# Kernel tuning notes

Hardware: AMD Instinct MI355X
Metric: run time of the kernel (lower is better)

Reference implementation:

```python
import jax, jax.numpy as jnp
import numpy as np

DIM = 64
NUM_NODES = 64
SEQ_LEN = 256
BATCH = 64


def setup_inputs() -> dict:
    key = jax.random.key(0)
    ks = jax.random.split(key, 8)
    D = DIM
    x = jax.random.normal(ks[0], (SEQ_LEN, BATCH, NUM_NODES, D), dtype=jnp.float32)
    mask = jnp.ones((SEQ_LEN,), dtype=jnp.int32)
    # msg MLP: Linear(3D -> D) + GELU
    lim_msg = 1.0 / np.sqrt(3 * D)
    msg_W = jax.random.uniform(ks[1], (D, 3 * D), minval=-lim_msg, maxval=lim_msg, dtype=jnp.float32)
    msg_b = jax.random.uniform(ks[2], (D,), minval=-lim_msg, maxval=lim_msg, dtype=jnp.float32)
    # GRUCell(input=D, hidden=D); torch init U(-1/sqrt(hidden), 1/sqrt(hidden))
    lim_g = 1.0 / np.sqrt(D)
    W_ih = jax.random.uniform(ks[3], (3 * D, D), minval=-lim_g, maxval=lim_g, dtype=jnp.float32)
    W_hh = jax.random.uniform(ks[4], (3 * D, D), minval=-lim_g, maxval=lim_g, dtype=jnp.float32)
    b_ih = jax.random.uniform(ks[5], (3 * D,), minval=-lim_g, maxval=lim_g, dtype=jnp.float32)
    b_hh = jax.random.uniform(ks[6], (3 * D,), minval=-lim_g, maxval=lim_g, dtype=jnp.float32)
    # TimeEncode params
    basis_freq = jnp.asarray(1.0 / 10.0 ** np.linspace(0, 9, D), dtype=jnp.float32)
    phase = jnp.zeros((D,), dtype=jnp.float32)
    return {"x": x, "mask": mask, "msg_W": msg_W, "msg_b": msg_b,
            "W_ih": W_ih, "W_hh": W_hh, "b_ih": b_ih, "b_hh": b_hh,
            "basis_freq": basis_freq, "phase": phase}


def _forward(x, mask, msg_W, msg_b, W_ih, W_hh, b_ih, b_hh, basis_freq, phase):
    T, B, C, D = x.shape
    # TimeEncode: cos(t * freq + phase) -> [T, D]
    ts = jnp.arange(T, dtype=jnp.float32)[:, None]
    t_enc = jnp.cos(ts * basis_freq[None, :] + phase[None, :])
    # init_func == 'mean': mean over time -> [B, C, D] -> [B*C, D]
    s0 = jnp.mean(x, axis=0).reshape(B * C, D)
    # time_range = arange(T) * mask (gather indices)
    tr = jnp.arange(T) * mask.astype(jnp.int32)
    x_seq = x[tr].reshape(T, B * C, D)      # gathered timesteps
    te_seq = t_enc[tr]                       # [T, D]

    def step(s, inp):
        xt, tt = inp                        # xt: [B*C, D], tt: [D]
        tt_b = jnp.broadcast_to(tt[None, :], xt.shape)
        cat = jnp.concatenate([xt, s, tt_b], axis=-1)  # [B*C, 3D]
        msg = jax.nn.gelu(cat @ msg_W.T + msg_b, approximate=False)
        # GRUCell (torch gate order: r, z, n)
        gi = msg @ W_ih.T + b_ih
        gh = s @ W_hh.T + b_hh
        i_r, i_z, i_n = jnp.split(gi, 3, axis=-1)
        h_r, h_z, h_n = jnp.split(gh, 3, axis=-1)
        r = jax.nn.sigmoid(i_r + h_r)
        z = jax.nn.sigmoid(i_z + h_z)
        n = jnp.tanh(i_n + r * h_n)
        s_new = (1.0 - z) * n + z * s
        return s_new, s_new

    _, states = jax.lax.scan(step, s0, (x_seq, te_seq))
    return states.reshape(T, B, C, D)


def reference(x, mask, msg_W, msg_b, W_ih, W_hh, b_ih, b_hh, basis_freq, phase):
    return _forward(x, mask, msg_W, msg_b, W_ih, W_hh, b_ih, b_hh, basis_freq, phase)
```

## Files before the change

### kernel.cpp

```cpp
#include <hip/hip_runtime.h>
#include <math.h>

#define DD    64
#define TT    256
#define NROW  4096
#define BLK   512
#define GRID  256

typedef __attribute__((ext_vector_type(8))) short  short8;
typedef __attribute__((ext_vector_type(4))) float  f32x4;

#define BARRIER() do {                                        \
    asm volatile("s_waitcnt lgkmcnt(0)" ::: "memory");        \
    __builtin_amdgcn_sched_barrier(0);                        \
    __builtin_amdgcn_s_barrier();                             \
    __builtin_amdgcn_sched_barrier(0);                        \
  } while (0)

__device__ __forceinline__ unsigned short f2bf(float f) {
  unsigned u = __builtin_bit_cast(unsigned, f);
  u += 0x7fffu + ((u >> 16) & 1u);
  return (unsigned short)(u >> 16);
}

__device__ __forceinline__ unsigned long long pack4(f32x4 v) {
  return (unsigned long long)f2bf(v[0])
       | ((unsigned long long)f2bf(v[1]) << 16)
       | ((unsigned long long)f2bf(v[2]) << 32)
       | ((unsigned long long)f2bf(v[3]) << 48);
}

__device__ __forceinline__ short8 pack_frag(f32x4 a, f32x4 b) {
  short8 r;
  r[0] = (short)f2bf(a[0]); r[1] = (short)f2bf(a[1]);
  r[2] = (short)f2bf(a[2]); r[3] = (short)f2bf(a[3]);
  r[4] = (short)f2bf(b[0]); r[5] = (short)f2bf(b[1]);
  r[6] = (short)f2bf(b[2]); r[7] = (short)f2bf(b[3]);
  return r;
}

__device__ __forceinline__ short8 load_wfrag(const float* p) {
  f32x4 a = *(const f32x4*)p;
  f32x4 b = *(const f32x4*)(p + 4);
  return pack_frag(a, b);
}

__device__ __forceinline__ float fsigmoid(float x) {
  return __builtin_amdgcn_rcpf(1.0f + __expf(-x));
}
__device__ __forceinline__ float ftanh(float x) {
  return 1.0f - 2.0f * __builtin_amdgcn_rcpf(1.0f + __expf(2.0f * x));
}
__device__ __forceinline__ float ferf(float x) {
  float ax = fabsf(x);
  float t  = __builtin_amdgcn_rcpf(fmaf(0.3275911f, ax, 1.0f));
  float p  = fmaf(1.061405429f, t, -1.453152027f);
  p = fmaf(p, t, 1.421413741f);
  p = fmaf(p, t, -0.284496736f);
  p = fmaf(p, t, 0.254829592f);
  p = p * t;
  float y = 1.0f - p * __expf(-ax * ax);
  return copysignf(y, x);
}

__global__ void bias_kernel(const float* __restrict__ msg_W,
                            const float* __restrict__ msg_b,
                            const float* __restrict__ freq,
                            const float* __restrict__ phase,
                            float* __restrict__ bias_t) {
  __shared__ float teL[DD];
  const int t = blockIdx.x;
  const int j = threadIdx.x;
  teL[j] = cosf(fmaf((float)t, freq[j], phase[j]));
  __syncthreads();
  float acc = msg_b[j];
  const float* wrow = msg_W + j * 192 + 128;
  #pragma unroll 8
  for (int k = 0; k < DD; ++k) acc = fmaf(teL[k], wrow[k], acc);
  bias_t[t * DD + j] = acc;
}

__launch_bounds__(BLK, 1)
__global__ void scan8(const float* __restrict__ x,
                      const int*   __restrict__ mask,
                      const float* __restrict__ msg_W,
                      const float* __restrict__ W_ih,
                      const float* __restrict__ W_hh,
                      const float* __restrict__ b_ih,
                      const float* __restrict__ b_hh,
                      const float* __restrict__ bias_t,
                      float* __restrict__ out) {
  __shared__ alignas(16) unsigned short xs[16 * 72];
  __shared__ alignas(16) unsigned short ss[16 * 72];
  __shared__ alignas(16) unsigned short ms[16 * 72];
  __shared__ alignas(16) float s0a[16 * 68];
  __shared__ alignas(16) float ghl[16 * 260];
  __shared__ int tr_lds[TT];

  const int tid  = threadIdx.x;
  const int lane = tid & 63;
  const int wv   = tid >> 6;
  const int grp  = wv >> 2;
  const int w4   = wv & 3;
  const int col  = lane & 15;
  const int kh   = lane >> 4;
  const int n    = w4 * 16 + col;
  const int row0 = blockIdx.x * 16;

  if (tid < TT) tr_lds[tid] = tid * mask[tid];

  short8 wm[4], wi[3][2], wh[3][2];
  float bsum01[2] = {0.f, 0.f}, bih2 = 0.f, bhh2 = 0.f;
  if (grp == 0) {
    const float* mrow = msg_W + (size_t)n * 192;
    #pragma unroll
    for (int kf = 0; kf < 4; ++kf) wm[kf] = load_wfrag(mrow + kf * 32 + kh * 8);
    #pragma unroll
    for (int p = 0; p < 3; ++p) {
      const float* irow = W_ih + (size_t)(p * 64 + n) * 64;
      #pragma unroll
      for (int kf = 0; kf < 2; ++kf) wi[p][kf] = load_wfrag(irow + kf * 32 + kh * 8);
    }
    bsum01[0] = b_ih[n]      + b_hh[n];
    bsum01[1] = b_ih[64 + n] + b_hh[64 + n];
    bih2 = b_ih[128 + n];
    bhh2 = b_hh[128 + n];
  } else {
    #pragma unroll
    for (int p = 0; p < 3; ++p) {
      const float* hrow = W_hh + (size_t)(p * 64 + n) * 64;
      #pragma unroll
      for (int kf = 0; kf < 2; ++kf) wh[p][kf] = load_wfrag(hrow + kf * 32 + kh * 8);
    }
  }

  {
    const int half = tid >> 8, rem = tid & 255;
    const int fr = rem >> 4, fd = (rem & 15) * 4;
    const float* px = x + ((size_t)half * 128) * (NROW * DD)
                        + (size_t)(row0 + fr) * DD + fd;
    f32x4 acc = {0.f, 0.f, 0.f, 0.f};
    #pragma unroll 4
    for (int tl = 0; tl < 128; ++tl) {
      f32x4 v = *(const f32x4*)(px + (size_t)tl * (NROW * DD));
      acc += v;
    }
    float* dst = (half == 0) ? &s0a[(rem >> 4) * 68 + fd] : &ghl[rem * 4];
    *(f32x4*)dst = acc;
  }
  __syncthreads();
  if (tid < 256) {
    const int fr = tid >> 4, fd = (tid & 15) * 4;
    f32x4 a = *(const f32x4*)&s0a[fr * 68 + fd];
    f32x4 b = *(const f32x4*)&ghl[tid * 4];
    f32x4 m = (a + b) * (1.0f / 256.0f);
    *(f32x4*)&s0a[fr * 68 + fd] = m;
    *(unsigned long long*)&ss[fr * 72 + fd] = pack4(m);
    f32x4 xv0 = *(const f32x4*)(x + (size_t)(row0 + fr) * DD + fd);
    *(unsigned long long*)&xs[fr * 72 + fd] = pack4(xv0);
  }
  __syncthreads();

  float s_reg[4] = {0.f, 0.f, 0.f, 0.f};
  float btc = 0.f;
  if (grp == 0) {
    #pragma unroll
    for (int i = 0; i < 4; ++i) s_reg[i] = s0a[(kh * 4 + i) * 68 + n];
    btc = bias_t[n];
    __builtin_amdgcn_s_setprio(1);
  }

  const int t1  = tid & 255;
  const int fr1 = t1 >> 4;
  const int fd1 = (t1 & 15) * 4;

  f32x4 xvA = {0.f, 0.f, 0.f, 0.f}, xvB = {0.f, 0.f, 0.f, 0.f};
  if (grp == 1)
    xvA = *(const f32x4*)(x + ((size_t)tr_lds[1] * NROW + row0 + fr1) * DD + fd1);

  auto body = [&](int t, f32x4& xv_use, f32x4& xv_load) {
    if (grp == 0) {
      const unsigned short* ax = &xs[(lane & 15) * 72];
      const unsigned short* as = &ss[(lane & 15) * 72];
      short8 xa0 = *(const short8*)(ax + kh * 8);
      short8 xa1 = *(const short8*)(ax + 32 + kh * 8);
      short8 sa0 = *(const short8*)(as + kh * 8);
      short8 sa1 = *(const short8*)(as + 32 + kh * 8);
      float btn = 0.f;
      if (t + 1 < TT) btn = bias_t[tr_lds[t + 1] * DD + n];
      f32x4 amx = {0.f, 0.f, 0.f, 0.f};
      amx = __builtin_amdgcn_mfma_f32_16x16x32_bf16(xa0, wm[0], amx, 0, 0, 0);
      amx = __builtin_amdgcn_mfma_f32_16x16x32_bf16(xa1, wm[1], amx, 0, 0, 0);
      f32x4 ams = {0.f, 0.f, 0.f, 0.f};
      ams = __builtin_amdgcn_mfma_f32_16x16x32_bf16(sa0, wm[2], ams, 0, 0, 0);
      ams = __builtin_amdgcn_mfma_f32_16x16x32_bf16(sa1, wm[3], ams, 0, 0, 0);
      #pragma unroll
      for (int i = 0; i < 4; ++i) {
        float a = amx[i] + ams[i] + btc;
        float g = 0.5f * a * (1.0f + ferf(a * 0.70710678118654752f));
        ms[(kh * 4 + i) * 72 + n] = f2bf(g);
      }
      btc = btn;
    } else {
      const unsigned short* as = &ss[(lane & 15) * 72];
      short8 sa0 = *(const short8*)(as + kh * 8);
      short8 sa1 = *(const short8*)(as + 32 + kh * 8);
      f32x4 agh[3];
      #pragma unroll
      for (int p = 0; p < 3; ++p) {
        f32x4 c = {0.f, 0.f, 0.f, 0.f};
        c = __builtin_amdgcn_mfma_f32_16x16x32_bf16(sa0, wh[p][0], c, 0, 0, 0);
        c = __builtin_amdgcn_mfma_f32_16x16x32_bf16(sa1, wh[p][1], c, 0, 0, 0);
        agh[p] = c;
      }
      #pragma unroll
      for (int i = 0; i < 4; ++i) {
        f32x4 gv = { agh[0][i], agh[1][i], agh[2][i], 0.f };
        *(f32x4*)&ghl[(kh * 4 + i) * 260 + n * 4] = gv;
      }
      if (t > 0) {
        f32x4 ov = *(const f32x4*)&s0a[fr1 * 68 + fd1];
        *(f32x4*)(out + ((size_t)(t - 1) * NROW + row0 + fr1) * DD + fd1) = ov;
      }
      if (t + 2 < TT)
        xv_load = *(const f32x4*)(x + ((size_t)tr_lds[t + 2] * NROW + row0 + fr1) * DD + fd1);
    }
    BARRIER();

    if (grp == 0) {
      f32x4 gh4[4];
      #pragma unroll
      for (int i = 0; i < 4; ++i)
        gh4[i] = *(const f32x4*)&ghl[(kh * 4 + i) * 260 + n * 4];
      const unsigned short* am = &ms[(lane & 15) * 72];
      short8 ma0 = *(const short8*)(am + kh * 8);
      short8 ma1 = *(const short8*)(am + 32 + kh * 8);
      f32x4 agi[3];
      #pragma unroll
      for (int p = 0; p < 3; ++p) {
        f32x4 c = {0.f, 0.f, 0.f, 0.f};
        c = __builtin_amdgcn_mfma_f32_16x16x32_bf16(ma0, wi[p][0], c, 0, 0, 0);
        c = __builtin_amdgcn_mfma_f32_16x16x32_bf16(ma1, wi[p][1], c, 0, 0, 0);
        agi[p] = c;
      }
      #pragma unroll
      for (int i = 0; i < 4; ++i) {
        const int rr = kh * 4 + i;
        float gr  = agi[0][i] + gh4[i][0] + bsum01[0];
        float gz  = agi[1][i] + gh4[i][1] + bsum01[1];
        float gni = agi[2][i] + bih2;
        float gnh = gh4[i][2] + bhh2;
        float rg = fsigmoid(gr);
        float zg = fsigmoid(gz);
        float ng = ftanh(fmaf(rg, gnh, gni));
        float sn = fmaf(zg, s_reg[i] - ng, ng);
        s_reg[i] = sn;
        ss[rr * 72 + n]  = f2bf(sn);
        s0a[rr * 68 + n] = sn;
      }
    } else {
      if (t + 1 < TT)
        *(unsigned long long*)&xs[fr1 * 72 + fd1] = pack4(xv_use);
    }
    BARRIER();
  };

  for (int tt = 0; tt < TT; tt += 2) {
    body(tt,     xvA, xvB);
    body(tt + 1, xvB, xvA);
  }

  if (grp == 1) {
    f32x4 ov = *(const f32x4*)&s0a[fr1 * 68 + fd1];
    *(f32x4*)(out + ((size_t)(TT - 1) * NROW + row0 + fr1) * DD + fd1) = ov;
  }
}

extern "C" void kernel_launch(void* const* d_in, const int* in_sizes, int n_in,
                              void* d_out, int out_size, void* d_ws, size_t ws_size,
                              hipStream_t stream) {
  const float* x      = (const float*)d_in[0];
  const int*   mask   = (const int*)  d_in[1];
  const float* msg_W  = (const float*)d_in[2];
  const float* msg_b  = (const float*)d_in[3];
  const float* W_ih   = (const float*)d_in[4];
  const float* W_hh   = (const float*)d_in[5];
  const float* b_ih   = (const float*)d_in[6];
  const float* b_hh   = (const float*)d_in[7];
  const float* freq   = (const float*)d_in[8];
  const float* phase  = (const float*)d_in[9];
  float* out    = (float*)d_out;
  float* bias_t = (float*)d_ws;

  (void)in_sizes; (void)n_in; (void)out_size; (void)ws_size;

  bias_kernel<<<TT, DD, 0, stream>>>(msg_W, msg_b, freq, phase, bias_t);
  scan8<<<GRID, BLK, 0, stream>>>(x, mask, msg_W, W_ih, W_hh,
                                  b_ih, b_hh, bias_t, out);
}
```

Baseline: 311.3 us.

## Merge warp groups into single 4-wave block and fold exp scaling into weights

Replaces the two specialised wave groups (message/GRU-input waves and hidden-projection waves) with a single group of four waves that computes all matmuls per step. This removes the ghl LDS exchange of hidden gates and the s0a staging buffer, and output is written directly from registers. GRU weights and biases are pre-scaled by -log2(e) or 2*log2(e) so sigmoid and tanh use a raw v_exp_f32, and erf also uses exp2 via inline asm. The trade-off is that each wave now issues more MFMA and transcendental work on the serial critical path, with no overlap between groups, in exchange for fewer LDS round trips per step.

```diff
diff --git a/kernel.cpp b/kernel.cpp
--- a/kernel.cpp
+++ b/kernel.cpp
@@ -4,7 +4,7 @@
 #define DD    64
 #define TT    256
 #define NROW  4096
-#define BLK   512
+#define BLK   256
 #define GRID  256
 
 typedef __attribute__((ext_vector_type(8))) short  short8;
@@ -16,6 +16,12 @@
     __builtin_amdgcn_s_barrier();                             \
     __builtin_amdgcn_sched_barrier(0);                        \
   } while (0)
+
+__device__ __forceinline__ float fexp2(float x) {
+  float r;
+  asm("v_exp_f32 %0, %1" : "=v"(r) : "v"(x));
+  return r;
+}
 
 __device__ __forceinline__ unsigned short f2bf(float f) {
   unsigned u = __builtin_bit_cast(unsigned, f);
@@ -45,12 +51,12 @@
   return pack_frag(a, b);
 }
 
-__device__ __forceinline__ float fsigmoid(float x) {
-  return __builtin_amdgcn_rcpf(1.0f + __expf(-x));
-}
-__device__ __forceinline__ float ftanh(float x) {
-  return 1.0f - 2.0f * __builtin_amdgcn_rcpf(1.0f + __expf(2.0f * x));
-}
+__device__ __forceinline__ short8 load_wfrag_s(const float* p, float s) {
+  f32x4 a = *(const f32x4*)p * s;
+  f32x4 b = *(const f32x4*)(p + 4) * s;
+  return pack_frag(a, b);
+}
+
 __device__ __forceinline__ float ferf(float x) {
   float ax = fabsf(x);
   float t  = __builtin_amdgcn_rcpf(fmaf(0.3275911f, ax, 1.0f));
@@ -59,7 +65,7 @@
   p = fmaf(p, t, -0.284496736f);
   p = fmaf(p, t, 0.254829592f);
   p = p * t;
-  float y = 1.0f - p * __expf(-ax * ax);
+  float y = 1.0f - p * fexp2(ax * ax * -1.44269504f);
   return copysignf(y, x);
 }
 
@@ -81,7 +87,7 @@
 }
 
 __launch_bounds__(BLK, 1)
-__global__ void scan8(const float* __restrict__ x,
+__global__ void scan9(const float* __restrict__ x,
                       const int*   __restrict__ mask,
                       const float* __restrict__ msg_W,
                       const float* __restrict__ W_ih,
@@ -93,186 +99,140 @@
   __shared__ alignas(16) unsigned short xs[16 * 72];
   __shared__ alignas(16) unsigned short ss[16 * 72];
   __shared__ alignas(16) unsigned short ms[16 * 72];
-  __shared__ alignas(16) float s0a[16 * 68];
-  __shared__ alignas(16) float ghl[16 * 260];
+  __shared__ alignas(16) float s0t[16 * 68];
   __shared__ int tr_lds[TT];
 
   const int tid  = threadIdx.x;
   const int lane = tid & 63;
   const int wv   = tid >> 6;
-  const int grp  = wv >> 2;
-  const int w4   = wv & 3;
   const int col  = lane & 15;
   const int kh   = lane >> 4;
-  const int n    = w4 * 16 + col;
+  const int n    = wv * 16 + col;
   const int row0 = blockIdx.x * 16;
 
-  if (tid < TT) tr_lds[tid] = tid * mask[tid];
-
+  tr_lds[tid] = tid * mask[tid];
+
+  const float SC_RZ = -1.44269504f, SC_N = 2.88539008f;
   short8 wm[4], wi[3][2], wh[3][2];
-  float bsum01[2] = {0.f, 0.f}, bih2 = 0.f, bhh2 = 0.f;
-  if (grp == 0) {
+  {
     const float* mrow = msg_W + (size_t)n * 192;
     #pragma unroll
     for (int kf = 0; kf < 4; ++kf) wm[kf] = load_wfrag(mrow + kf * 32 + kh * 8);
+    const float sc[3] = {SC_RZ, SC_RZ, SC_N};
     #pragma unroll
     for (int p = 0; p < 3; ++p) {
       const float* irow = W_ih + (size_t)(p * 64 + n) * 64;
-      #pragma unroll
-      for (int kf = 0; kf < 2; ++kf) wi[p][kf] = load_wfrag(irow + kf * 32 + kh * 8);
-    }
-    bsum01[0] = b_ih[n]      + b_hh[n];
-    bsum01[1] = b_ih[64 + n] + b_hh[64 + n];
-    bih2 = b_ih[128 + n];
-    bhh2 = b_hh[128 + n];
-  } else {
-    #pragma unroll
-    for (int p = 0; p < 3; ++p) {
       const float* hrow = W_hh + (size_t)(p * 64 + n) * 64;
       #pragma unroll
-      for (int kf = 0; kf < 2; ++kf) wh[p][kf] = load_wfrag(hrow + kf * 32 + kh * 8);
+      for (int kf = 0; kf < 2; ++kf) {
+        wi[p][kf] = load_wfrag_s(irow + kf * 32 + kh * 8, sc[p]);
+        wh[p][kf] = load_wfrag_s(hrow + kf * 32 + kh * 8, sc[p]);
+      }
     }
   }
+  const float bsum0 = (b_ih[n]       + b_hh[n])       * SC_RZ;
+  const float bsum1 = (b_ih[64 + n]  + b_hh[64 + n])  * SC_RZ;
+  const float bih2  =  b_ih[128 + n] * SC_N;
+  const float bhh2  =  b_hh[128 + n] * SC_N;
+
+  const int fr = tid >> 4;
+  const int fd = (tid & 15) * 4;
 
   {
-    const int half = tid >> 8, rem = tid & 255;
-    const int fr = rem >> 4, fd = (rem & 15) * 4;
-    const float* px = x + ((size_t)half * 128) * (NROW * DD)
-                        + (size_t)(row0 + fr) * DD + fd;
-    f32x4 acc = {0.f, 0.f, 0.f, 0.f};
+    const float* px = x + (size_t)(row0 + fr) * DD + fd;
+    f32x4 a0 = {0.f,0.f,0.f,0.f}, a1 = {0.f,0.f,0.f,0.f};
     #pragma unroll 4
-    for (int tl = 0; tl < 128; ++tl) {
-      f32x4 v = *(const f32x4*)(px + (size_t)tl * (NROW * DD));
-      acc += v;
-    }
-    float* dst = (half == 0) ? &s0a[(rem >> 4) * 68 + fd] : &ghl[rem * 4];
-    *(f32x4*)dst = acc;
-  }
-  __syncthreads();
-  if (tid < 256) {
-    const int fr = tid >> 4, fd = (tid & 15) * 4;
-    f32x4 a = *(const f32x4*)&s0a[fr * 68 + fd];
-    f32x4 b = *(const f32x4*)&ghl[tid * 4];
-    f32x4 m = (a + b) * (1.0f / 256.0f);
-    *(f32x4*)&s0a[fr * 68 + fd] = m;
+    for (int t = 0; t < TT; t += 2) {
+      a0 += *(const f32x4*)(px + (size_t)t * (NROW * DD));
+      a1 += *(const f32x4*)(px + (size_t)(t + 1) * (NROW * DD));
+    }
+    f32x4 m = (a0 + a1) * (1.0f / 256.0f);
+    *(f32x4*)&s0t[fr * 68 + fd] = m;
     *(unsigned long long*)&ss[fr * 72 + fd] = pack4(m);
-    f32x4 xv0 = *(const f32x4*)(x + (size_t)(row0 + fr) * DD + fd);
+    f32x4 xv0 = *(const f32x4*)px;
     *(unsigned long long*)&xs[fr * 72 + fd] = pack4(xv0);
   }
   __syncthreads();
 
-  float s_reg[4] = {0.f, 0.f, 0.f, 0.f};
-  float btc = 0.f;
-  if (grp == 0) {
-    #pragma unroll
-    for (int i = 0; i < 4; ++i) s_reg[i] = s0a[(kh * 4 + i) * 68 + n];
-    btc = bias_t[n];
-    __builtin_amdgcn_s_setprio(1);
-  }
-
-  const int t1  = tid & 255;
-  const int fr1 = t1 >> 4;
-  const int fd1 = (t1 & 15) * 4;
-
-  f32x4 xvA = {0.f, 0.f, 0.f, 0.f}, xvB = {0.f, 0.f, 0.f, 0.f};
-  if (grp == 1)
-    xvA = *(const f32x4*)(x + ((size_t)tr_lds[1] * NROW + row0 + fr1) * DD + fd1);
+  float s_reg[4];
+  #pragma unroll
+  for (int i = 0; i < 4; ++i) s_reg[i] = s0t[(kh * 4 + i) * 68 + n];
+  float btc = bias_t[n];
+
+  f32x4 xvA = {0.f,0.f,0.f,0.f}, xvB = {0.f,0.f,0.f,0.f};
+  xvA = *(const f32x4*)(x + ((size_t)tr_lds[1] * NROW + row0 + fr) * DD + fd);
 
   auto body = [&](int t, f32x4& xv_use, f32x4& xv_load) {
-    if (grp == 0) {
-      const unsigned short* ax = &xs[(lane & 15) * 72];
-      const unsigned short* as = &ss[(lane & 15) * 72];
-      short8 xa0 = *(const short8*)(ax + kh * 8);
-      short8 xa1 = *(const short8*)(ax + 32 + kh * 8);
-      short8 sa0 = *(const short8*)(as + kh * 8);
-      short8 sa1 = *(const short8*)(as + 32 + kh * 8);
-      float btn = 0.f;
-      if (t + 1 < TT) btn = bias_t[tr_lds[t + 1] * DD + n];
-      f32x4 amx = {0.f, 0.f, 0.f, 0.f};
-      amx = __builtin_amdgcn_mfma_f32_16x16x32_bf16(xa0, wm[0], amx, 0, 0, 0);
-      amx = __builtin_amdgcn_mfma_f32_16x16x32_bf16(xa1, wm[1], amx, 0, 0, 0);
-      f32x4 ams = {0.f, 0.f, 0.f, 0.f};
-      ams = __builtin_amdgcn_mfma_f32_16x16x32_bf16(sa0, wm[2], ams, 0, 0, 0);
-      ams = __builtin_amdgcn_mfma_f32_16x16x32_bf16(sa1, wm[3], ams, 0, 0, 0);
-      #pragma unroll
-      for (int i = 0; i < 4; ++i) {
-        float a = amx[i] + ams[i] + btc;
-        float g = 0.5f * a * (1.0f + ferf(a * 0.70710678118654752f));
-        ms[(kh * 4 + i) * 72 + n] = f2bf(g);
-      }
-      btc = btn;
-    } else {
-      const unsigned short* as = &ss[(lane & 15) * 72];
-      short8 sa0 = *(const short8*)(as + kh * 8);
-      short8 sa1 = *(const short8*)(as + 32 + kh * 8);
-      f32x4 agh[3];
-      #pragma unroll
-      for (int p = 0; p < 3; ++p) {
-        f32x4 c = {0.f, 0.f, 0.f, 0.f};
-        c = __builtin_amdgcn_mfma_f32_16x16x32_bf16(sa0, wh[p][0], c, 0, 0, 0);
-        c = __builtin_amdgcn_mfma_f32_16x16x32_bf16(sa1, wh[p][1], c, 0, 0, 0);
-        agh[p] = c;
-      }
-      #pragma unroll
-      for (int i = 0; i < 4; ++i) {
-        f32x4 gv = { agh[0][i], agh[1][i], agh[2][i], 0.f };
-        *(f32x4*)&ghl[(kh * 4 + i) * 260 + n * 4] = gv;
-      }
-      if (t > 0) {
-        f32x4 ov = *(const f32x4*)&s0a[fr1 * 68 + fd1];
-        *(f32x4*)(out + ((size_t)(t - 1) * NROW + row0 + fr1) * DD + fd1) = ov;
-      }
-      if (t + 2 < TT)
-        xv_load = *(const f32x4*)(x + ((size_t)tr_lds[t + 2] * NROW + row0 + fr1) * DD + fd1);
-    }
+    if (t + 2 < TT)
+      xv_load = *(const f32x4*)(x + ((size_t)tr_lds[t + 2] * NROW + row0 + fr) * DD + fd);
+    float btn = 0.f;
+    if (t + 1 < TT) btn = bias_t[tr_lds[t + 1] * DD + n];
+
+    const unsigned short* ax = &xs[(lane & 15) * 72];
+    const unsigned short* as = &ss[(lane & 15) * 72];
+    short8 xa0 = *(const short8*)(ax + kh * 8);
+    short8 xa1 = *(const short8*)(ax + 32 + kh * 8);
+    short8 sa0 = *(const short8*)(as + kh * 8);
+    short8 sa1 = *(const short8*)(as + 32 + kh * 8);
+
+    f32x4 amx = {0.f,0.f,0.f,0.f};
+    amx = __builtin_amdgcn_mfma_f32_16x16x32_bf16(xa0, wm[0], amx, 0, 0, 0);
+    amx = __builtin_amdgcn_mfma_f32_16x16x32_bf16(xa1, wm[1], amx, 0, 0, 0);
+    f32x4 ams = {0.f,0.f,0.f,0.f};
+    ams = __builtin_amdgcn_mfma_f32_16x16x32_bf16(sa0, wm[2], ams, 0, 0, 0);
+    ams = __builtin_amdgcn_mfma_f32_16x16x32_bf16(sa1, wm[3], ams, 0, 0, 0);
+    f32x4 agh[3];
+    #pragma unroll
+    for (int p = 0; p < 3; ++p) {
+      f32x4 c = {0.f,0.f,0.f,0.f};
+      c = __builtin_amdgcn_mfma_f32_16x16x32_bf16(sa0, wh[p][0], c, 0, 0, 0);
+      c = __builtin_amdgcn_mfma_f32_16x16x32_bf16(sa1, wh[p][1], c, 0, 0, 0);
+      agh[p] = c;
+    }
+
+    #pragma unroll
+    for (int i = 0; i < 4; ++i) {
+      float a = amx[i] + ams[i] + btc;
+      float g = 0.5f * a * (1.0f + ferf(a * 0.70710678118654752f));
+      ms[(kh * 4 + i) * 72 + n] = f2bf(g);
+    }
+    btc = btn;
     BARRIER();
 
-    if (grp == 0) {
-      f32x4 gh4[4];
-      #pragma unroll
-      for (int i = 0; i < 4; ++i)
-        gh4[i] = *(const f32x4*)&ghl[(kh * 4 + i) * 260 + n * 4];
-      const unsigned short* am = &ms[(lane & 15) * 72];
-      short8 ma0 = *(const short8*)(am + kh * 8);
-      short8 ma1 = *(const short8*)(am + 32 + kh * 8);
-      f32x4 agi[3];
-      #pragma unroll
-      for (int p = 0; p < 3; ++p) {
-        f32x4 c = {0.f, 0.f, 0.f, 0.f};
-        c = __builtin_amdgcn_mfma_f32_16x16x32_bf16(ma0, wi[p][0], c, 0, 0, 0);
-        c = __builtin_amdgcn_mfma_f32_16x16x32_bf16(ma1, wi[p][1], c, 0, 0, 0);
-        agi[p] = c;
-      }
-      #pragma unroll
-      for (int i = 0; i < 4; ++i) {
-        const int rr = kh * 4 + i;
-        float gr  = agi[0][i] + gh4[i][0] + bsum01[0];
-        float gz  = agi[1][i] + gh4[i][1] + bsum01[1];
-        float gni = agi[2][i] + bih2;
-        float gnh = gh4[i][2] + bhh2;
-        float rg = fsigmoid(gr);
-        float zg = fsigmoid(gz);
-        float ng = ftanh(fmaf(rg, gnh, gni));
-        float sn = fmaf(zg, s_reg[i] - ng, ng);
-        s_reg[i] = sn;
-        ss[rr * 72 + n]  = f2bf(sn);
-        s0a[rr * 68 + n] = sn;
-      }
-    } else {
-      if (t + 1 < TT)
-        *(unsigned long long*)&xs[fr1 * 72 + fd1] = pack4(xv_use);
-    }
+    const unsigned short* am = &ms[(lane & 15) * 72];
+    short8 ma0 = *(const short8*)(am + kh * 8);
+    short8 ma1 = *(const short8*)(am + 32 + kh * 8);
+    f32x4 agi[3];
+    #pragma unroll
+    for (int p = 0; p < 3; ++p) {
+      f32x4 c = {0.f,0.f,0.f,0.f};
+      c = __builtin_amdgcn_mfma_f32_16x16x32_bf16(ma0, wi[p][0], c, 0, 0, 0);
+      c = __builtin_amdgcn_mfma_f32_16x16x32_bf16(ma1, wi[p][1], c, 0, 0, 0);
+      agi[p] = c;
+    }
+
+    #pragma unroll
+    for (int i = 0; i < 4; ++i) {
+      const int rr = kh * 4 + i;
+      float er = agi[0][i] + agh[0][i] + bsum0;
+      float ez = agi[1][i] + agh[1][i] + bsum1;
+      float rg = __builtin_amdgcn_rcpf(1.0f + fexp2(er));
+      float zg = __builtin_amdgcn_rcpf(1.0f + fexp2(ez));
+      float yn = fmaf(rg, agh[2][i] + bhh2, agi[2][i] + bih2);
+      float ng = 1.0f - 2.0f * __builtin_amdgcn_rcpf(1.0f + fexp2(yn));
+      float sn = fmaf(zg, s_reg[i] - ng, ng);
+      s_reg[i] = sn;
+      ss[rr * 72 + n] = f2bf(sn);
+      out[((size_t)t * NROW + row0 + rr) * DD + n] = sn;
+    }
+    if (t + 1 < TT)
+      *(unsigned long long*)&xs[fr * 72 + fd] = pack4(xv_use);
     BARRIER();
   };
 
   for (int tt = 0; tt < TT; tt += 2) {
     body(tt,     xvA, xvB);
     body(tt + 1, xvB, xvA);
-  }
-
-  if (grp == 1) {
-    f32x4 ov = *(const f32x4*)&s0a[fr1 * 68 + fd1];
-    *(f32x4*)(out + ((size_t)(TT - 1) * NROW + row0 + fr1) * DD + fd1) = ov;
   }
 }
 
@@ -295,6 +255,6 @@
   (void)in_sizes; (void)n_in; (void)out_size; (void)ws_size;
 
   bias_kernel<<<TT, DD, 0, stream>>>(msg_W, msg_b, freq, phase, bias_t);
-  scan8<<<GRID, BLK, 0, stream>>>(x, mask, msg_W, W_ih, W_hh,
+  scan9<<<GRID, BLK, 0, stream>>>(x, mask, msg_W, W_ih, W_hh,
                                   b_ih, b_hh, bias_t, out);
 }
```

Result: slower. 360.4 us (+15.8%).

## Load x fragments directly into MFMA waves and fold exp scaling into GRU weights

Applied to the files above, without the earlier changes.

The MLP-side waves now load their own x fragments from global memory two steps ahead and pack them in registers. This removes the xs LDS staging buffer and the extra store by the other wave group in the second phase. GRU weights and biases are pre-scaled by -log2(e) or 2·log2(e) so the sigmoid and tanh use raw v_exp_f32 without a multiply. Float-to-bf16 conversion uses the hardware v_cvt_pk_bf16_f32 instruction instead of integer rounding. The trade-off is more global loads and registers on the critical-path wave group, plus different rounding from pre-scaling weights in bf16.

```diff
diff --git a/kernel.cpp b/kernel.cpp
--- a/kernel.cpp
+++ b/kernel.cpp
@@ -17,40 +17,41 @@
     __builtin_amdgcn_sched_barrier(0);                        \
   } while (0)
 
-__device__ __forceinline__ unsigned short f2bf(float f) {
-  unsigned u = __builtin_bit_cast(unsigned, f);
-  u += 0x7fffu + ((u >> 16) & 1u);
-  return (unsigned short)(u >> 16);
-}
-
+__device__ __forceinline__ float fexp2(float x) {
+  float r;
+  asm("v_exp_f32 %0, %1" : "=v"(r) : "v"(x));
+  return r;
+}
+
+__device__ __forceinline__ unsigned cvtpk(float lo, float hi) {
+  unsigned r;
+  asm("v_cvt_pk_bf16_f32 %0, %1, %2" : "=v"(r) : "v"(lo), "v"(hi));
+  return r;
+}
+__device__ __forceinline__ unsigned short f2bf1(float f) {
+  return (unsigned short)cvtpk(f, f);
+}
 __device__ __forceinline__ unsigned long long pack4(f32x4 v) {
-  return (unsigned long long)f2bf(v[0])
-       | ((unsigned long long)f2bf(v[1]) << 16)
-       | ((unsigned long long)f2bf(v[2]) << 32)
-       | ((unsigned long long)f2bf(v[3]) << 48);
-}
-
+  unsigned lo = cvtpk(v[0], v[1]), hi = cvtpk(v[2], v[3]);
+  return (unsigned long long)lo | ((unsigned long long)hi << 32);
+}
 __device__ __forceinline__ short8 pack_frag(f32x4 a, f32x4 b) {
-  short8 r;
-  r[0] = (short)f2bf(a[0]); r[1] = (short)f2bf(a[1]);
-  r[2] = (short)f2bf(a[2]); r[3] = (short)f2bf(a[3]);
-  r[4] = (short)f2bf(b[0]); r[5] = (short)f2bf(b[1]);
-  r[6] = (short)f2bf(b[2]); r[7] = (short)f2bf(b[3]);
-  return r;
-}
-
+  union { unsigned u[4]; short8 s; } z;
+  z.u[0] = cvtpk(a[0], a[1]); z.u[1] = cvtpk(a[2], a[3]);
+  z.u[2] = cvtpk(b[0], b[1]); z.u[3] = cvtpk(b[2], b[3]);
+  return z.s;
+}
 __device__ __forceinline__ short8 load_wfrag(const float* p) {
   f32x4 a = *(const f32x4*)p;
   f32x4 b = *(const f32x4*)(p + 4);
   return pack_frag(a, b);
 }
-
-__device__ __forceinline__ float fsigmoid(float x) {
-  return __builtin_amdgcn_rcpf(1.0f + __expf(-x));
-}
-__device__ __forceinline__ float ftanh(float x) {
-  return 1.0f - 2.0f * __builtin_amdgcn_rcpf(1.0f + __expf(2.0f * x));
-}
+__device__ __forceinline__ short8 load_wfrag_s(const float* p, float s) {
+  f32x4 a = *(const f32x4*)p * s;
+  f32x4 b = *(const f32x4*)(p + 4) * s;
+  return pack_frag(a, b);
+}
+
 __device__ __forceinline__ float ferf(float x) {
   float ax = fabsf(x);
   float t  = __builtin_amdgcn_rcpf(fmaf(0.3275911f, ax, 1.0f));
@@ -59,7 +60,7 @@
   p = fmaf(p, t, -0.284496736f);
   p = fmaf(p, t, 0.254829592f);
   p = p * t;
-  float y = 1.0f - p * __expf(-ax * ax);
+  float y = 1.0f - p * fexp2(ax * ax * -1.44269504f);
   return copysignf(y, x);
 }
 
@@ -81,16 +82,15 @@
 }
 
 __launch_bounds__(BLK, 1)
-__global__ void scan8(const float* __restrict__ x,
-                      const int*   __restrict__ mask,
-                      const float* __restrict__ msg_W,
-                      const float* __restrict__ W_ih,
-                      const float* __restrict__ W_hh,
-                      const float* __restrict__ b_ih,
-                      const float* __restrict__ b_hh,
-                      const float* __restrict__ bias_t,
-                      float* __restrict__ out) {
-  __shared__ alignas(16) unsigned short xs[16 * 72];
+__global__ void scan10(const float* __restrict__ x,
+                       const int*   __restrict__ mask,
+                       const float* __restrict__ msg_W,
+                       const float* __restrict__ W_ih,
+                       const float* __restrict__ W_hh,
+                       const float* __restrict__ b_ih,
+                       const float* __restrict__ b_hh,
+                       const float* __restrict__ bias_t,
+                       float* __restrict__ out) {
   __shared__ alignas(16) unsigned short ss[16 * 72];
   __shared__ alignas(16) unsigned short ms[16 * 72];
   __shared__ alignas(16) float s0a[16 * 68];
@@ -105,32 +105,38 @@
   const int col  = lane & 15;
   const int kh   = lane >> 4;
   const int n    = w4 * 16 + col;
+  const int r16  = lane & 15;
   const int row0 = blockIdx.x * 16;
 
   if (tid < TT) tr_lds[tid] = tid * mask[tid];
 
+  const float SC_RZ = -1.44269504f, SC_N = 2.88539008f;
   short8 wm[4], wi[3][2], wh[3][2];
-  float bsum01[2] = {0.f, 0.f}, bih2 = 0.f, bhh2 = 0.f;
+  float bsum0 = 0.f, bsum1 = 0.f, bih2 = 0.f, bhh2 = 0.f;
   if (grp == 0) {
     const float* mrow = msg_W + (size_t)n * 192;
     #pragma unroll
     for (int kf = 0; kf < 4; ++kf) wm[kf] = load_wfrag(mrow + kf * 32 + kh * 8);
+    const float sc[3] = {SC_RZ, SC_RZ, SC_N};
     #pragma unroll
     for (int p = 0; p < 3; ++p) {
       const float* irow = W_ih + (size_t)(p * 64 + n) * 64;
       #pragma unroll
-      for (int kf = 0; kf < 2; ++kf) wi[p][kf] = load_wfrag(irow + kf * 32 + kh * 8);
-    }
-    bsum01[0] = b_ih[n]      + b_hh[n];
-    bsum01[1] = b_ih[64 + n] + b_hh[64 + n];
-    bih2 = b_ih[128 + n];
-    bhh2 = b_hh[128 + n];
+      for (int kf = 0; kf < 2; ++kf)
+        wi[p][kf] = load_wfrag_s(irow + kf * 32 + kh * 8, sc[p]);
+    }
+    bsum0 = (b_ih[n]      + b_hh[n])      * SC_RZ;
+    bsum1 = (b_ih[64 + n] + b_hh[64 + n]) * SC_RZ;
+    bih2  =  b_ih[128 + n] * SC_N;
+    bhh2  =  b_hh[128 + n] * SC_N;
   } else {
+    const float sc[3] = {SC_RZ, SC_RZ, SC_N};
     #pragma unroll
     for (int p = 0; p < 3; ++p) {
       const float* hrow = W_hh + (size_t)(p * 64 + n) * 64;
       #pragma unroll
-      for (int kf = 0; kf < 2; ++kf) wh[p][kf] = load_wfrag(hrow + kf * 32 + kh * 8);
+      for (int kf = 0; kf < 2; ++kf)
+        wh[p][kf] = load_wfrag_s(hrow + kf * 32 + kh * 8, sc[p]);
     }
   }
 
@@ -145,7 +151,7 @@
       f32x4 v = *(const f32x4*)(px + (size_t)tl * (NROW * DD));
       acc += v;
     }
-    float* dst = (half == 0) ? &s0a[(rem >> 4) * 68 + fd] : &ghl[rem * 4];
+    float* dst = (half == 0) ? &s0a[fr * 68 + fd] : &ghl[rem * 4];
     *(f32x4*)dst = acc;
   }
   __syncthreads();
@@ -156,17 +162,23 @@
     f32x4 m = (a + b) * (1.0f / 256.0f);
     *(f32x4*)&s0a[fr * 68 + fd] = m;
     *(unsigned long long*)&ss[fr * 72 + fd] = pack4(m);
-    f32x4 xv0 = *(const f32x4*)(x + (size_t)(row0 + fr) * DD + fd);
-    *(unsigned long long*)&xs[fr * 72 + fd] = pack4(xv0);
   }
   __syncthreads();
 
   float s_reg[4] = {0.f, 0.f, 0.f, 0.f};
   float btc = 0.f;
+  f32x4 xA0 = {0,0,0,0}, xA1 = {0,0,0,0}, xA2 = {0,0,0,0}, xA3 = {0,0,0,0};
+  f32x4 xB0 = {0,0,0,0}, xB1 = {0,0,0,0}, xB2 = {0,0,0,0}, xB3 = {0,0,0,0};
   if (grp == 0) {
     #pragma unroll
     for (int i = 0; i < 4; ++i) s_reg[i] = s0a[(kh * 4 + i) * 68 + n];
     btc = bias_t[n];
+    const float* p0 = x + (size_t)(row0 + r16) * DD + kh * 8;
+    xA0 = *(const f32x4*)p0;       xA1 = *(const f32x4*)(p0 + 4);
+    xA2 = *(const f32x4*)(p0 + 32); xA3 = *(const f32x4*)(p0 + 36);
+    const float* p1 = x + ((size_t)tr_lds[1] * NROW + row0 + r16) * DD + kh * 8;
+    xB0 = *(const f32x4*)p1;       xB1 = *(const f32x4*)(p1 + 4);
+    xB2 = *(const f32x4*)(p1 + 32); xB3 = *(const f32x4*)(p1 + 36);
     __builtin_amdgcn_s_setprio(1);
   }
 
@@ -174,41 +186,41 @@
   const int fr1 = t1 >> 4;
   const int fd1 = (t1 & 15) * 4;
 
-  f32x4 xvA = {0.f, 0.f, 0.f, 0.f}, xvB = {0.f, 0.f, 0.f, 0.f};
-  if (grp == 1)
-    xvA = *(const f32x4*)(x + ((size_t)tr_lds[1] * NROW + row0 + fr1) * DD + fd1);
-
-  auto body = [&](int t, f32x4& xv_use, f32x4& xv_load) {
+  auto body = [&](int t, f32x4& v0, f32x4& v1, f32x4& v2, f32x4& v3) {
     if (grp == 0) {
-      const unsigned short* ax = &xs[(lane & 15) * 72];
-      const unsigned short* as = &ss[(lane & 15) * 72];
-      short8 xa0 = *(const short8*)(ax + kh * 8);
-      short8 xa1 = *(const short8*)(ax + 32 + kh * 8);
+      short8 xa0 = pack_frag(v0, v1);
+      short8 xa1 = pack_frag(v2, v3);
+      f32x4 amx = {0.f,0.f,0.f,0.f};
+      amx = __builtin_amdgcn_mfma_f32_16x16x32_bf16(xa0, wm[0], amx, 0, 0, 0);
+      amx = __builtin_amdgcn_mfma_f32_16x16x32_bf16(xa1, wm[1], amx, 0, 0, 0);
+      if (t + 2 < TT) {
+        const float* pn = x + ((size_t)tr_lds[t + 2] * NROW + row0 + r16) * DD + kh * 8;
+        v0 = *(const f32x4*)pn;        v1 = *(const f32x4*)(pn + 4);
+        v2 = *(const f32x4*)(pn + 32); v3 = *(const f32x4*)(pn + 36);
+      }
+      float btn = 0.f;
+      if (t + 1 < TT) btn = bias_t[tr_lds[t + 1] * DD + n];
+      const unsigned short* as = &ss[r16 * 72];
       short8 sa0 = *(const short8*)(as + kh * 8);
       short8 sa1 = *(const short8*)(as + 32 + kh * 8);
-      float btn = 0.f;
-      if (t + 1 < TT) btn = bias_t[tr_lds[t + 1] * DD + n];
-      f32x4 amx = {0.f, 0.f, 0.f, 0.f};
-      amx = __builtin_amdgcn_mfma_f32_16x16x32_bf16(xa0, wm[0], amx, 0, 0, 0);
-      amx = __builtin_amdgcn_mfma_f32_16x16x32_bf16(xa1, wm[1], amx, 0, 0, 0);
-      f32x4 ams = {0.f, 0.f, 0.f, 0.f};
+      f32x4 ams = {0.f,0.f,0.f,0.f};
       ams = __builtin_amdgcn_mfma_f32_16x16x32_bf16(sa0, wm[2], ams, 0, 0, 0);
       ams = __builtin_amdgcn_mfma_f32_16x16x32_bf16(sa1, wm[3], ams, 0, 0, 0);
       #pragma unroll
       for (int i = 0; i < 4; ++i) {
         float a = amx[i] + ams[i] + btc;
         float g = 0.5f * a * (1.0f + ferf(a * 0.70710678118654752f));
-        ms[(kh * 4 + i) * 72 + n] = f2bf(g);
+        ms[(kh * 4 + i) * 72 + n] = f2bf1(g);
       }
       btc = btn;
     } else {
-      const unsigned short* as = &ss[(lane & 15) * 72];
+      const unsigned short* as = &ss[r16 * 72];
       short8 sa0 = *(const short8*)(as + kh * 8);
       short8 sa1 = *(const short8*)(as + 32 + kh * 8);
       f32x4 agh[3];
       #pragma unroll
       for (int p = 0; p < 3; ++p) {
-        f32x4 c = {0.f, 0.f, 0.f, 0.f};
+        f32x4 c = {0.f,0.f,0.f,0.f};
         c = __builtin_amdgcn_mfma_f32_16x16x32_bf16(sa0, wh[p][0], c, 0, 0, 0);
         c = __builtin_amdgcn_mfma_f32_16x16x32_bf16(sa1, wh[p][1], c, 0, 0, 0);
         agh[p] = c;
@@ -222,8 +234,6 @@
         f32x4 ov = *(const f32x4*)&s0a[fr1 * 68 + fd1];
         *(f32x4*)(out + ((size_t)(t - 1) * NROW + row0 + fr1) * DD + fd1) = ov;
       }
-      if (t + 2 < TT)
-        xv_load = *(const f32x4*)(x + ((size_t)tr_lds[t + 2] * NROW + row0 + fr1) * DD + fd1);
     }
     BARRIER();
 
@@ -232,13 +242,13 @@
       #pragma unroll
       for (int i = 0; i < 4; ++i)
         gh4[i] = *(const f32x4*)&ghl[(kh * 4 + i) * 260 + n * 4];
-      const unsigned short* am = &ms[(lane & 15) * 72];
+      const unsigned short* am = &ms[r16 * 72];
       short8 ma0 = *(const short8*)(am + kh * 8);
       short8 ma1 = *(const short8*)(am + 32 + kh * 8);
       f32x4 agi[3];
       #pragma unroll
       for (int p = 0; p < 3; ++p) {
-        f32x4 c = {0.f, 0.f, 0.f, 0.f};
+        f32x4 c = {0.f,0.f,0.f,0.f};
         c = __builtin_amdgcn_mfma_f32_16x16x32_bf16(ma0, wi[p][0], c, 0, 0, 0);
         c = __builtin_amdgcn_mfma_f32_16x16x32_bf16(ma1, wi[p][1], c, 0, 0, 0);
         agi[p] = c;
@@ -246,28 +256,24 @@
       #pragma unroll
       for (int i = 0; i < 4; ++i) {
         const int rr = kh * 4 + i;
-        float gr  = agi[0][i] + gh4[i][0] + bsum01[0];
-        float gz  = agi[1][i] + gh4[i][1] + bsum01[1];
-        float gni = agi[2][i] + bih2;
-        float gnh = gh4[i][2] + bhh2;
-        float rg = fsigmoid(gr);
-        float zg = fsigmoid(gz);
-        float ng = ftanh(fmaf(rg, gnh, gni));
+        float er = agi[0][i] + gh4[i][0] + bsum0;
+        float ez = agi[1][i] + gh4[i][1] + bsum1;
+        float rg = __builtin_amdgcn_rcpf(1.0f + fexp2(er));
+        float zg = __builtin_amdgcn_rcpf(1.0f + fexp2(ez));
+        float yn = fmaf(rg, gh4[i][2] + bhh2, agi[2][i] + bih2);
+        float ng = 1.0f - 2.0f * __builtin_amdgcn_rcpf(1.0f + fexp2(yn));
         float sn = fmaf(zg, s_reg[i] - ng, ng);
         s_reg[i] = sn;
-        ss[rr * 72 + n]  = f2bf(sn);
+        ss[rr * 72 + n]  = f2bf1(sn);
         s0a[rr * 68 + n] = sn;
       }
-    } else {
-      if (t + 1 < TT)
-        *(unsigned long long*)&xs[fr1 * 72 + fd1] = pack4(xv_use);
     }
     BARRIER();
   };
 
   for (int tt = 0; tt < TT; tt += 2) {
-    body(tt,     xvA, xvB);
-    body(tt + 1, xvB, xvA);
+    body(tt,     xA0, xA1, xA2, xA3);
+    body(tt + 1, xB0, xB1, xB2, xB3);
   }
 
   if (grp == 1) {
@@ -295,6 +301,6 @@
   (void)in_sizes; (void)n_in; (void)out_size; (void)ws_size;
 
   bias_kernel<<<TT, DD, 0, stream>>>(msg_W, msg_b, freq, phase, bias_t);
-  scan8<<<GRID, BLK, 0, stream>>>(x, mask, msg_W, W_ih, W_hh,
-                                  b_ih, b_hh, bias_t, out);
-}
+  scan10<<<GRID, BLK, 0, stream>>>(x, mask, msg_W, W_ih, W_hh,
+                                   b_ih, b_hh, bias_t, out);
+}
```

New measurement: 443.9 us. 1.43x slower.
